# Optimization experiments

Measured on AMD Instinct MI355X. Metric: run time of the kernel, lower is better.

## Reference

```python
import jax, jax.numpy as jnp
import numpy as np

N = 100000   # nodes
E = 3200000  # edges (avg degree 32)
D = 128      # input feature dim


def setup_inputs() -> dict:
    key = jax.random.key(0)
    ks = jax.random.split(key, 9)
    x = jax.random.normal(ks[0], (N, D), dtype=jnp.float32)
    edge_index = jax.random.randint(ks[1], (2, E), 0, N, dtype=jnp.int32)
    s = 0.05
    W1 = jax.random.normal(ks[2], (D, 64), dtype=jnp.float32) * s
    b1 = jnp.zeros((64,), dtype=jnp.float32)
    W2 = jax.random.normal(ks[3], (64, 32), dtype=jnp.float32) * s
    b2 = jnp.zeros((32,), dtype=jnp.float32)
    Wfc = jax.random.normal(ks[4], (32, 1), dtype=jnp.float32) * s
    bfc = jnp.zeros((1,), dtype=jnp.float32)
    return {"x": x, "edge_index": edge_index, "W1": W1, "b1": b1,
            "W2": W2, "b2": b2, "Wfc": Wfc, "bfc": bfc}


def _gcn_layer(x, W, b, src, dst, n):
    # GCNConv: h = D^{-1/2} (A + I) D^{-1/2} (x W) + b
    h = x @ W  # [n, out]
    loop = jnp.arange(n, dtype=src.dtype)
    src2 = jnp.concatenate([src, loop])  # add self-loops
    dst2 = jnp.concatenate([dst, loop])
    deg = jax.ops.segment_sum(jnp.ones_like(dst2, dtype=h.dtype), dst2,
                              num_segments=n)  # >= 1 due to self-loops
    dis = jax.lax.rsqrt(deg)
    norm = dis[src2] * dis[dst2]  # [E+n]
    msgs = h[src2] * norm[:, None]  # gather + scale
    return jax.ops.segment_sum(msgs, dst2, num_segments=n) + b


def reference(x, edge_index, W1, b1, W2, b2, Wfc, bfc):
    src, dst = edge_index[0], edge_index[1]
    n = x.shape[0]
    h = jax.nn.relu(_gcn_layer(x, W1, b1, src, dst, n))
    h = jax.nn.relu(_gcn_layer(h, W2, b2, src, dst, n))
    return h @ Wfc + bfc  # [n, 1]
```

## Files before the change

kernel.cpp:

```cpp
#include <hip/hip_runtime.h>
#include <hip/hip_bf16.h>
#include <hip/hip_fp16.h>


#define SCAN_CHUNK 1024
#define BSHIFT 7
#define BSIZE 128
#define B1 256
#define CSR_CAP 5120

__device__ inline void f4fma(float4& a, float s, const float4& b) {
    a.x = fmaf(s, b.x, a.x); a.y = fmaf(s, b.y, a.y);
    a.z = fmaf(s, b.z, a.z); a.w = fmaf(s, b.w, a.w);
}
__device__ inline void f4add(float4& a, const float4& b) {
    a.x += b.x; a.y += b.y; a.z += b.z; a.w += b.w;
}
__device__ inline void f4red(float4& a, int off) {
    a.x += __shfl_xor(a.x, off); a.y += __shfl_xor(a.y, off);
    a.z += __shfl_xor(a.z, off); a.w += __shfl_xor(a.w, off);
}
__device__ inline void h8load(const __half* p, float4& a, float4& b) {
    uint4 r = *(const uint4*)p;
    __half2* h = (__half2*)&r;
    float2 f0 = __half22float2(h[0]);
    float2 f1 = __half22float2(h[1]);
    float2 f2 = __half22float2(h[2]);
    float2 f3 = __half22float2(h[3]);
    a = make_float4(f0.x, f0.y, f1.x, f1.y);
    b = make_float4(f2.x, f2.y, f3.x, f3.y);
}
__device__ inline void hacc2(unsigned h, float& x, float& y) {
    asm("v_fma_mix_f32 %0, %2, %3, %0 op_sel:[0,0,0] op_sel_hi:[1,0,0]\n\t"
        "v_fma_mix_f32 %1, %2, %3, %1 op_sel:[1,0,0] op_sel_hi:[1,0,0]"
        : "+v"(x), "+v"(y)
        : "v"(h), "v"(1.0f));
}
__device__ inline void h8acc(const __half* p, float4& a, float4& b) {
    uint4 r = *(const uint4*)p;
    hacc2(r.x, a.x, a.y);
    hacc2(r.y, a.z, a.w);
    hacc2(r.z, b.x, b.y);
    hacc2(r.w, b.z, b.w);
}
__device__ inline void h4store(__half* p, float4 v) {
    __half2 a = __floats2half2_rn(v.x, v.y);
    __half2 b = __floats2half2_rn(v.z, v.w);
    uint2 r; r.x = *(uint*)&a; r.y = *(uint*)&b;
    *(uint2*)p = r;
}

__global__ void k_gscan1(const int* __restrict__ in, int* __restrict__ part, int m) {
    int t = threadIdx.x;
    int base = blockIdx.x * SCAN_CHUNK + t * 4;
    int s = 0;
    for (int u = 0; u < 4; ++u) { int i = base + u; if (i < m) s += in[i]; }
    for (int o = 32; o; o >>= 1) s += __shfl_down(s, o);
    __shared__ int ws[4];
    if ((t & 63) == 0) ws[t >> 6] = s;
    __syncthreads();
    if (t == 0) part[blockIdx.x] = ws[0] + ws[1] + ws[2] + ws[3];
}

__global__ void k_gscan2(const int* __restrict__ in, const int* __restrict__ part,
                         int* __restrict__ out, int m, int nblk) {
    int t = threadIdx.x;
    int b = blockIdx.x;
    int pv = (t < b && t < nblk) ? part[t] : 0;
    int ps = pv;
    for (int o = 32; o; o >>= 1) ps += __shfl_down(ps, o);
    __shared__ int sh[4];
    if ((t & 63) == 0) sh[t >> 6] = ps;
    __syncthreads();
    int blockoff = sh[0] + sh[1] + sh[2] + sh[3];

    int base = b * SCAN_CHUNK + t * 4;
    int v0 = 0, v1 = 0, v2 = 0, v3 = 0;
    if (base + 0 < m) v0 = in[base + 0];
    if (base + 1 < m) v1 = in[base + 1];
    if (base + 2 < m) v2 = in[base + 2];
    if (base + 3 < m) v3 = in[base + 3];
    int tot = v0 + v1 + v2 + v3;
    int lane = t & 63, wid = t >> 6;
    int incl = tot;
    for (int o = 1; o < 64; o <<= 1) { int u = __shfl_up(incl, o); if (lane >= o) incl += u; }
    int excl = incl - tot;
    __shared__ int wt[4];
    if (lane == 63) wt[wid] = incl;
    __syncthreads();
    int woff = 0;
    for (int w = 0; w < wid; ++w) woff += wt[w];
    int off = blockoff + woff + excl;
    if (base + 0 < m) out[base + 0] = off;
    if (base + 1 < m) out[base + 1] = off + v0;
    if (base + 2 < m) out[base + 2] = off + v0 + v1;
    if (base + 3 < m) out[base + 3] = off + v0 + v1 + v2;
}

__global__ __launch_bounds__(256) void k_hist(const int* __restrict__ dst,
                                              int* __restrict__ ghist,
                                              int e, int echunk, int nbuck) {
    extern __shared__ int h[];
    int t = threadIdx.x, b = blockIdx.x;
    for (int i = t; i < nbuck; i += 256) h[i] = 0;
    __syncthreads();
    int s = b * echunk, epd = min(e, s + echunk);
    for (int i = s + t * 4; i < epd; i += 1024) {
        if (i + 3 < epd) {
            int4 d4 = *(const int4*)&dst[i];
            atomicAdd(&h[d4.x >> BSHIFT], 1);
            atomicAdd(&h[d4.y >> BSHIFT], 1);
            atomicAdd(&h[d4.z >> BSHIFT], 1);
            atomicAdd(&h[d4.w >> BSHIFT], 1);
        } else {
            for (int u = i; u < epd; ++u) atomicAdd(&h[dst[u] >> BSHIFT], 1);
        }
    }
    __syncthreads();
    for (int k = t; k < nbuck; k += 256)
        ghist[k * B1 + b] = h[k];
}

__global__ __launch_bounds__(256) void k_binscatter(
        const int* __restrict__ src, const int* __restrict__ dst,
        const int* __restrict__ ghist_s, int* __restrict__ ebuf,
        int e, int echunk, int nbuck) {
    extern __shared__ int cur[];
    int t = threadIdx.x, b = blockIdx.x;
    for (int k = t; k < nbuck; k += 256)
        cur[k] = ghist_s[k * B1 + b];
    __syncthreads();
    int s = b * echunk, epd = min(e, s + echunk);
    for (int i = s + t * 4; i < epd; i += 1024) {
        if (i + 3 < epd) {
            int4 d4 = *(const int4*)&dst[i];
            int4 s4 = *(const int4*)&src[i];
            int p0 = atomicAdd(&cur[d4.x >> BSHIFT], 1);
            int p1 = atomicAdd(&cur[d4.y >> BSHIFT], 1);
            int p2 = atomicAdd(&cur[d4.z >> BSHIFT], 1);
            int p3 = atomicAdd(&cur[d4.w >> BSHIFT], 1);
            ebuf[p0] = (s4.x << BSHIFT) | (d4.x & (BSIZE - 1));
            ebuf[p1] = (s4.y << BSHIFT) | (d4.y & (BSIZE - 1));
            ebuf[p2] = (s4.z << BSHIFT) | (d4.z & (BSIZE - 1));
            ebuf[p3] = (s4.w << BSHIFT) | (d4.w & (BSIZE - 1));
        } else {
            for (int u = i; u < epd; ++u) {
                int d = dst[u];
                int pos = atomicAdd(&cur[d >> BSHIFT], 1);
                ebuf[pos] = (src[u] << BSHIFT) | (d & (BSIZE - 1));
            }
        }
    }
}

__global__ __launch_bounds__(256) void k_csr(
        const int* __restrict__ ebuf, const int* __restrict__ ghist_s,
        int* __restrict__ ebuf2, int* __restrict__ rowptr, int* __restrict__ degi,
        float* __restrict__ dis, int n, int e, int nbuck) {
    int k = blockIdx.x, t = threadIdx.x;
    int estart = ghist_s[k * B1];
    int eend = (k + 1 < nbuck) ? ghist_s[(k + 1) * B1] : e;
    int ecnt = eend - estart;
    __shared__ int ein[CSR_CAP];
    __shared__ int eout[CSR_CAP];
    __shared__ int cnt[BSIZE];
    __shared__ int cur[BSIZE];
    __shared__ int wt[4];
    if (t < BSIZE) cnt[t] = 0;
    bool staged = (ecnt <= CSR_CAP);
    if (staged) {
        for (int i = t; i < ecnt; i += 256) ein[i] = ebuf[estart + i];
    }
    __syncthreads();
    if (staged) {
        for (int i = t; i < ecnt; i += 256)
            atomicAdd(&cnt[ein[i] & (BSIZE - 1)], 1);
    } else {
        for (int i = estart + t; i < eend; i += 256)
            atomicAdd(&cnt[ebuf[i] & (BSIZE - 1)], 1);
    }
    __syncthreads();
    int v = (t < BSIZE) ? cnt[t] : 0;
    int lane = t & 63, wid = t >> 6;
    int incl = v;
    for (int o = 1; o < 64; o <<= 1) { int u = __shfl_up(incl, o); if (lane >= o) incl += u; }
    if (lane == 63) wt[wid] = incl;
    __syncthreads();
    int woff = (wid == 1) ? wt[0] : 0;
    int excl = woff + incl - v;
    if (t < BSIZE) {
        cur[t] = excl;
        int node = k * BSIZE + t;
        if (node < n) {
            rowptr[node] = estart + excl;
            degi[node]   = v;
            dis[node]    = rsqrtf((float)(v + 1));
        }
    }
    __syncthreads();
    if (staged) {
        for (int i = t; i < ecnt; i += 256) {
            int w = ein[i];
            int pos = atomicAdd(&cur[w & (BSIZE - 1)], 1);
            eout[pos] = w;
        }
        __syncthreads();
        for (int i = t; i < ecnt; i += 256)
            ebuf2[estart + i] = eout[i];
    } else {
        for (int i = estart + t; i < eend; i += 256) {
            int w = ebuf[i];
            int pos = estart + atomicAdd(&cur[w & (BSIZE - 1)], 1);
            ebuf2[pos] = w;
        }
    }
}

#define SA 132
__global__ __launch_bounds__(256) void k_gemm1(
        const float* __restrict__ x, const float* __restrict__ W1,
        const float* __restrict__ dis, __half* __restrict__ h1s, int n) {
    __shared__ float Xs[64 * SA];
    __shared__ float Ws[128 * 64];
    int t = threadIdx.x;
    int nbase = blockIdx.x * 64;
    for (int i = t; i < 2048; i += 256)
        ((float4*)Ws)[i] = ((const float4*)W1)[i];
    for (int i = t; i < 2048; i += 256) {
        int row = i >> 5, q = i & 31;
        int r = nbase + row; if (r >= n) r = n - 1;
        float4 v = ((const float4*)(x + (size_t)r * 128))[q];
        *(float4*)&Xs[row * SA + q * 4] = v;
    }
    __syncthreads();
    int wid = t >> 6, lane = t & 63;
    int lx = lane & 7, ly = lane >> 3;
    int wm = wid & 1, wn = wid >> 1;
    int row0 = wm * 32 + ly * 4;
    int col0 = wn * 32 + lx * 4;
    float4 acc0 = {0.f,0.f,0.f,0.f}, acc1 = acc0, acc2 = acc0, acc3 = acc0;
#pragma unroll 4
    for (int k4 = 0; k4 < 32; ++k4) {
        int k = k4 * 4;
        float4 a0 = *(const float4*)&Xs[(row0 + 0) * SA + k];
        float4 a1 = *(const float4*)&Xs[(row0 + 1) * SA + k];
        float4 a2 = *(const float4*)&Xs[(row0 + 2) * SA + k];
        float4 a3 = *(const float4*)&Xs[(row0 + 3) * SA + k];
        float4 b0 = *(const float4*)&Ws[(k + 0) * 64 + col0];
        float4 b1 = *(const float4*)&Ws[(k + 1) * 64 + col0];
        float4 b2 = *(const float4*)&Ws[(k + 2) * 64 + col0];
        float4 b3 = *(const float4*)&Ws[(k + 3) * 64 + col0];
        f4fma(acc0, a0.x, b0); f4fma(acc0, a0.y, b1); f4fma(acc0, a0.z, b2); f4fma(acc0, a0.w, b3);
        f4fma(acc1, a1.x, b0); f4fma(acc1, a1.y, b1); f4fma(acc1, a1.z, b2); f4fma(acc1, a1.w, b3);
        f4fma(acc2, a2.x, b0); f4fma(acc2, a2.y, b1); f4fma(acc2, a2.z, b2); f4fma(acc2, a2.w, b3);
        f4fma(acc3, a3.x, b0); f4fma(acc3, a3.y, b1); f4fma(acc3, a3.z, b2); f4fma(acc3, a3.w, b3);
    }
    int grow = nbase + row0;
#pragma unroll
    for (int r = 0; r < 4; ++r) {
        int rr = grow + r;
        if (rr < n) {
            float d = dis[rr];
            float4 o = (r == 0) ? acc0 : (r == 1) ? acc1 : (r == 2) ? acc2 : acc3;
            o.x *= d; o.y *= d; o.z *= d; o.w *= d;
            h4store(&h1s[(size_t)rr * 64 + col0], o);
        }
    }
}

__global__ __launch_bounds__(256) void k_agg12(
        const __half* __restrict__ h1s, const int* __restrict__ ents,
        const int* __restrict__ rowptr, const int* __restrict__ degi,
        const float* __restrict__ dis, const float* __restrict__ b1,
        const float* __restrict__ W2, __half* __restrict__ h2s, int n) {
    __shared__ float h1row[4][72];
    int wid = threadIdx.x >> 6, lane = threadIdx.x & 63;
    int v = blockIdx.x * 4 + wid;
    int vc = min(v, n - 1);
    int start = rowptr[vc], cnt = degi[vc];
    int eg = lane >> 3;
    int fq = (lane & 7) * 8;
    int c = lane & 31, hh = lane >> 5;
    float w2r[32];
#pragma unroll
    for (int j = 0; j < 32; ++j)
        w2r[j] = W2[(hh * 32 + j) * 32 + c];
    float4 accA = {0.f, 0.f, 0.f, 0.f}, accB = accA;
    if (cnt > 0 && cnt <= 64) {
        int pre = ents[start + min(lane, cnt - 1)];
        int ng = cnt >> 3;
#pragma unroll 4
        for (int g = 0; g < ng; ++g) {
            unsigned s = ((unsigned)__shfl(pre, g * 8 + eg)) >> BSHIFT;
            h8acc(&h1s[(size_t)s * 64 + fq], accA, accB);
        }
        int rem = cnt & 7, j0 = cnt & ~7;
        if (rem) {
            unsigned s = ((unsigned)__shfl(pre, j0 + (eg < rem ? eg : 0))) >> BSHIFT;
            float4 a, b; h8load(&h1s[(size_t)s * 64 + fq], a, b);
            if (eg < rem) { f4add(accA, a); f4add(accB, b); }
        }
    } else if (cnt > 64) {
        int j = 0;
        for (; j + 8 <= cnt; j += 8) {
            unsigned s = ((unsigned)ents[start + j + eg]) >> BSHIFT;
            h8acc(&h1s[(size_t)s * 64 + fq], accA, accB);
        }
        int rem = cnt - j;
        if (rem) {
            unsigned s = ((unsigned)ents[start + j + (eg < rem ? eg : 0)]) >> BSHIFT;
            float4 a, b; h8load(&h1s[(size_t)s * 64 + fq], a, b);
            if (eg < rem) { f4add(accA, a); f4add(accB, b); }
        }
    }
    if (eg == 0) {
        h8acc(&h1s[(size_t)vc * 64 + fq], accA, accB);
    }
    f4red(accA, 8);  f4red(accB, 8);
    f4red(accA, 16); f4red(accB, 16);
    f4red(accA, 32); f4red(accB, 32);
    float d = dis[vc];
    if (eg == 0) {
        float4 bq0 = *(const float4*)&b1[fq];
        float4 bq1 = *(const float4*)&b1[fq + 4];
        float4 o0, o1;
        o0.x = fmaxf(fmaf(d, accA.x, bq0.x), 0.f);
        o0.y = fmaxf(fmaf(d, accA.y, bq0.y), 0.f);
        o0.z = fmaxf(fmaf(d, accA.z, bq0.z), 0.f);
        o0.w = fmaxf(fmaf(d, accA.w, bq0.w), 0.f);
        o1.x = fmaxf(fmaf(d, accB.x, bq1.x), 0.f);
        o1.y = fmaxf(fmaf(d, accB.y, bq1.y), 0.f);
        o1.z = fmaxf(fmaf(d, accB.z, bq1.z), 0.f);
        o1.w = fmaxf(fmaf(d, accB.w, bq1.w), 0.f);
        *(float4*)&h1row[wid][fq] = o0;
        *(float4*)&h1row[wid][fq + 4] = o1;
    }
    __syncthreads();
    float p = 0.f;
#pragma unroll
    for (int j = 0; j < 32; j += 4) {
        float4 hv = *(const float4*)&h1row[wid][hh * 32 + j];
        p = fmaf(hv.x, w2r[j + 0], p);
        p = fmaf(hv.y, w2r[j + 1], p);
        p = fmaf(hv.z, w2r[j + 2], p);
        p = fmaf(hv.w, w2r[j + 3], p);
    }
    p += __shfl_xor(p, 32);
    if (hh == 0 && v < n) h2s[(size_t)v * 32 + c] = __float2half(p * d);
}

__global__ void k_agg2(const __half* __restrict__ h2s, const int* __restrict__ ents,
                       const int* __restrict__ rowptr, const int* __restrict__ degi,
                       const float* __restrict__ dis, const float* __restrict__ b2,
                       const float* __restrict__ Wfc, const float* __restrict__ bfc,
                       float* __restrict__ out, int n) {
    int wid = threadIdx.x >> 6, lane = threadIdx.x & 63;
    int v = blockIdx.x * 4 + wid;
    if (v >= n) return;
    int start = rowptr[v], cnt = degi[v];
    int eg = lane >> 2;
    int fq = (lane & 3) * 8;
    float4 accA = {0.f, 0.f, 0.f, 0.f}, accB = accA;
    if (cnt > 0 && cnt <= 64) {
        int pre = ents[start + min(lane, cnt - 1)];
        int ng = cnt >> 4;
#pragma unroll 4
        for (int g = 0; g < ng; ++g) {
            unsigned s = ((unsigned)__shfl(pre, g * 16 + eg)) >> BSHIFT;
            h8acc(&h2s[(size_t)s * 32 + fq], accA, accB);
        }
        int rem = cnt & 15, j0 = cnt & ~15;
        if (rem) {
            unsigned s = ((unsigned)__shfl(pre, j0 + (eg < rem ? eg : 0))) >> BSHIFT;
            float4 a, b; h8load(&h2s[(size_t)s * 32 + fq], a, b);
            if (eg < rem) { f4add(accA, a); f4add(accB, b); }
        }
    } else if (cnt > 64) {
        int j = 0;
        for (; j + 16 <= cnt; j += 16) {
            unsigned s = ((unsigned)ents[start + j + eg]) >> BSHIFT;
            h8acc(&h2s[(size_t)s * 32 + fq], accA, accB);
        }
        int rem = cnt - j;
        if (rem) {
            unsigned s = ((unsigned)ents[start + j + (eg < rem ? eg : 0)]) >> BSHIFT;
            float4 a, b; h8load(&h2s[(size_t)s * 32 + fq], a, b);
            if (eg < rem) { f4add(accA, a); f4add(accB, b); }
        }
    }
    if (eg == 0) {
        h8acc(&h2s[(size_t)v * 32 + fq], accA, accB);
    }
    f4red(accA, 4);  f4red(accB, 4);
    f4red(accA, 8);  f4red(accB, 8);
    f4red(accA, 16); f4red(accB, 16);
    f4red(accA, 32); f4red(accB, 32);
    float p = 0.f;
    if (eg == 0) {
        float d = dis[v];
        float4 bq0 = *(const float4*)&b2[fq];
        float4 bq1 = *(const float4*)&b2[fq + 4];
        float4 wq0 = *(const float4*)&Wfc[fq];
        float4 wq1 = *(const float4*)&Wfc[fq + 4];
        p  = fmaxf(fmaf(d, accA.x, bq0.x), 0.f) * wq0.x;
        p += fmaxf(fmaf(d, accA.y, bq0.y), 0.f) * wq0.y;
        p += fmaxf(fmaf(d, accA.z, bq0.z), 0.f) * wq0.z;
        p += fmaxf(fmaf(d, accA.w, bq0.w), 0.f) * wq0.w;
        p += fmaxf(fmaf(d, accB.x, bq1.x), 0.f) * wq1.x;
        p += fmaxf(fmaf(d, accB.y, bq1.y), 0.f) * wq1.y;
        p += fmaxf(fmaf(d, accB.z, bq1.z), 0.f) * wq1.z;
        p += fmaxf(fmaf(d, accB.w, bq1.w), 0.f) * wq1.w;
    }
    p += __shfl_xor(p, 1); p += __shfl_xor(p, 2);
    if (lane == 0) out[v] = p + bfc[0];
}

extern "C" void kernel_launch(void* const* d_in, const int* in_sizes, int n_in,
                              void* d_out, int out_size, void* d_ws, size_t ws_size,
                              hipStream_t stream) {
    const float* x   = (const float*)d_in[0];
    const int*   ei  = (const int*)d_in[1];
    const float* W1  = (const float*)d_in[2];
    const float* b1  = (const float*)d_in[3];
    const float* W2  = (const float*)d_in[4];
    const float* b2  = (const float*)d_in[5];
    const float* Wfc = (const float*)d_in[6];
    const float* bfc = (const float*)d_in[7];
    float* out = (float*)d_out;

    const int n = in_sizes[0] / 128;
    const int e = in_sizes[1] / 2;
    const int* src = ei;
    const int* dst = ei + e;

    const int nbuck = (n + BSIZE - 1) / BSIZE;
    const int m = nbuck * B1;
    const int echunk = (e + B1 - 1) / B1;

    char* p = (char*)d_ws;
    size_t off = 0;
    auto carve = [&](size_t bytes) { void* r = p + off; off = (off + bytes + 255) & ~(size_t)255; return r; };
    int*   ghist   = (int*)  carve((size_t)m * 4);
    int*   ghist_s = (int*)  carve((size_t)m * 4);
    int*   part    = (int*)  carve(256 * 4);
    float* dis     = (float*)carve((size_t)n * 4);
    int*   rowptr  = (int*)  carve((size_t)n * 4);
    int*   degi    = (int*)  carve((size_t)n * 4);
    int*   ebuf2   = (int*)  carve((size_t)e * 4);
    __half* h2s    = (__half*)carve((size_t)n * 32 * 2);
    void*  ebuf_or_h1s = carve((size_t)e * 4);
    int*    ebuf = (int*)ebuf_or_h1s;
    __half* h1s  = (__half*)ebuf_or_h1s;
    (void)ws_size;

    const int nblk_scan = (m + SCAN_CHUNK - 1) / SCAN_CHUNK;
    const size_t lds_buck = (size_t)nbuck * 4;

    k_hist<<<B1, 256, lds_buck, stream>>>(dst, ghist, e, echunk, nbuck);
    k_gscan1<<<nblk_scan, 256, 0, stream>>>(ghist, part, m);
    k_gscan2<<<nblk_scan, 256, 0, stream>>>(ghist, part, ghist_s, m, nblk_scan);
    k_binscatter<<<B1, 256, lds_buck, stream>>>(src, dst, ghist_s, ebuf, e, echunk, nbuck);
    k_csr<<<nbuck, 256, 0, stream>>>(ebuf, ghist_s, ebuf2, rowptr, degi, dis, n, e, nbuck);
    k_gemm1<<<(n + 63) / 64, 256, 0, stream>>>(x, W1, dis, h1s, n);
    k_agg12<<<(n + 3) / 4, 256, 0, stream>>>(h1s, ebuf2, rowptr, degi, dis, b1, W2, h2s, n);
    k_agg2<<<(n + 3) / 4, 256, 0, stream>>>(h2s, ebuf2, rowptr, degi, dis, b2, Wfc, bfc, out, n);
}
```

Baseline: 305.6 us.

## Replace bucketed two-pass CSR build with global atomic degree count and scatter

Removes the LDS-bucketed histogram, bin-scatter and per-bucket CSR sort kernels. In their place it counts per-node degree with global atomics, scans it directly into rowptr, cursors and dis, and scatters source ids into CSR slots with global atomics. Entries now hold plain source ids, so the aggregation kernels drop the shift decode, and W2 is pre-transposed so agg12 can load its weights as vectorized float4. This cuts kernel count and passes over the edges but relies on heavily contended global atomics with random destinations and gives a nondeterministic neighbor order within each row.

Measured after the change: 699.0 us. +128.7%, slower.

```diff
diff --git a/kernel.cpp b/kernel.cpp
--- a/kernel.cpp
+++ b/kernel.cpp
@@ -4,10 +4,6 @@
 
 
 #define SCAN_CHUNK 1024
-#define BSHIFT 7
-#define BSIZE 128
-#define B1 256
-#define CSR_CAP 5120
 
 __device__ inline void f4fma(float4& a, float s, const float4& b) {
     a.x = fmaf(s, b.x, a.x); a.y = fmaf(s, b.y, a.y);
@@ -50,6 +46,28 @@
     *(uint2*)p = r;
 }
 
+__global__ __launch_bounds__(256) void k_deg(const int* __restrict__ dst,
+                                             int* __restrict__ deg,
+                                             const float* __restrict__ W2,
+                                             float* __restrict__ W2T, int e) {
+    int tid = blockIdx.x * 256 + threadIdx.x;
+    int i = tid * 4;
+    int stride = gridDim.x * 1024;
+    for (; i + 3 < e; i += stride) {
+        int4 d4 = *(const int4*)&dst[i];
+        atomicAdd(&deg[d4.x], 1);
+        atomicAdd(&deg[d4.y], 1);
+        atomicAdd(&deg[d4.z], 1);
+        atomicAdd(&deg[d4.w], 1);
+    }
+    for (int u = (e & ~3) + tid; u < e; u += gridDim.x * 256)
+        atomicAdd(&deg[dst[u]], 1);
+    if (blockIdx.x == 0) {
+        for (int j = threadIdx.x; j < 2048; j += 256)
+            W2T[j] = W2[(j & 63) * 32 + (j >> 6)];
+    }
+}
+
 __global__ void k_gscan1(const int* __restrict__ in, int* __restrict__ part, int m) {
     int t = threadIdx.x;
     int base = blockIdx.x * SCAN_CHUNK + t * 4;
@@ -63,7 +81,8 @@
 }
 
 __global__ void k_gscan2(const int* __restrict__ in, const int* __restrict__ part,
-                         int* __restrict__ out, int m, int nblk) {
+                         int* __restrict__ rowptr, int* __restrict__ cur,
+                         float* __restrict__ dis, int m, int nblk) {
     int t = threadIdx.x;
     int b = blockIdx.x;
     int pv = (t < b && t < nblk) ? part[t] : 0;
@@ -91,129 +110,28 @@
     int woff = 0;
     for (int w = 0; w < wid; ++w) woff += wt[w];
     int off = blockoff + woff + excl;
-    if (base + 0 < m) out[base + 0] = off;
-    if (base + 1 < m) out[base + 1] = off + v0;
-    if (base + 2 < m) out[base + 2] = off + v0 + v1;
-    if (base + 3 < m) out[base + 3] = off + v0 + v1 + v2;
-}
-
-__global__ __launch_bounds__(256) void k_hist(const int* __restrict__ dst,
-                                              int* __restrict__ ghist,
-                                              int e, int echunk, int nbuck) {
-    extern __shared__ int h[];
-    int t = threadIdx.x, b = blockIdx.x;
-    for (int i = t; i < nbuck; i += 256) h[i] = 0;
-    __syncthreads();
-    int s = b * echunk, epd = min(e, s + echunk);
-    for (int i = s + t * 4; i < epd; i += 1024) {
-        if (i + 3 < epd) {
-            int4 d4 = *(const int4*)&dst[i];
-            atomicAdd(&h[d4.x >> BSHIFT], 1);
-            atomicAdd(&h[d4.y >> BSHIFT], 1);
-            atomicAdd(&h[d4.z >> BSHIFT], 1);
-            atomicAdd(&h[d4.w >> BSHIFT], 1);
-        } else {
-            for (int u = i; u < epd; ++u) atomicAdd(&h[dst[u] >> BSHIFT], 1);
-        }
-    }
-    __syncthreads();
-    for (int k = t; k < nbuck; k += 256)
-        ghist[k * B1 + b] = h[k];
-}
-
-__global__ __launch_bounds__(256) void k_binscatter(
+    if (base + 0 < m) { rowptr[base+0] = off;          cur[base+0] = off;          dis[base+0] = rsqrtf((float)(v0+1)); }
+    if (base + 1 < m) { int o1 = off+v0;               rowptr[base+1] = o1; cur[base+1] = o1; dis[base+1] = rsqrtf((float)(v1+1)); }
+    if (base + 2 < m) { int o2 = off+v0+v1;            rowptr[base+2] = o2; cur[base+2] = o2; dis[base+2] = rsqrtf((float)(v2+1)); }
+    if (base + 3 < m) { int o3 = off+v0+v1+v2;         rowptr[base+3] = o3; cur[base+3] = o3; dis[base+3] = rsqrtf((float)(v3+1)); }
+}
+
+__global__ __launch_bounds__(256) void k_scatter(
         const int* __restrict__ src, const int* __restrict__ dst,
-        const int* __restrict__ ghist_s, int* __restrict__ ebuf,
-        int e, int echunk, int nbuck) {
-    extern __shared__ int cur[];
-    int t = threadIdx.x, b = blockIdx.x;
-    for (int k = t; k < nbuck; k += 256)
-        cur[k] = ghist_s[k * B1 + b];
-    __syncthreads();
-    int s = b * echunk, epd = min(e, s + echunk);
-    for (int i = s + t * 4; i < epd; i += 1024) {
-        if (i + 3 < epd) {
-            int4 d4 = *(const int4*)&dst[i];
-            int4 s4 = *(const int4*)&src[i];
-            int p0 = atomicAdd(&cur[d4.x >> BSHIFT], 1);
-            int p1 = atomicAdd(&cur[d4.y >> BSHIFT], 1);
-            int p2 = atomicAdd(&cur[d4.z >> BSHIFT], 1);
-            int p3 = atomicAdd(&cur[d4.w >> BSHIFT], 1);
-            ebuf[p0] = (s4.x << BSHIFT) | (d4.x & (BSIZE - 1));
-            ebuf[p1] = (s4.y << BSHIFT) | (d4.y & (BSIZE - 1));
-            ebuf[p2] = (s4.z << BSHIFT) | (d4.z & (BSIZE - 1));
-            ebuf[p3] = (s4.w << BSHIFT) | (d4.w & (BSIZE - 1));
-        } else {
-            for (int u = i; u < epd; ++u) {
-                int d = dst[u];
-                int pos = atomicAdd(&cur[d >> BSHIFT], 1);
-                ebuf[pos] = (src[u] << BSHIFT) | (d & (BSIZE - 1));
-            }
-        }
-    }
-}
-
-__global__ __launch_bounds__(256) void k_csr(
-        const int* __restrict__ ebuf, const int* __restrict__ ghist_s,
-        int* __restrict__ ebuf2, int* __restrict__ rowptr, int* __restrict__ degi,
-        float* __restrict__ dis, int n, int e, int nbuck) {
-    int k = blockIdx.x, t = threadIdx.x;
-    int estart = ghist_s[k * B1];
-    int eend = (k + 1 < nbuck) ? ghist_s[(k + 1) * B1] : e;
-    int ecnt = eend - estart;
-    __shared__ int ein[CSR_CAP];
-    __shared__ int eout[CSR_CAP];
-    __shared__ int cnt[BSIZE];
-    __shared__ int cur[BSIZE];
-    __shared__ int wt[4];
-    if (t < BSIZE) cnt[t] = 0;
-    bool staged = (ecnt <= CSR_CAP);
-    if (staged) {
-        for (int i = t; i < ecnt; i += 256) ein[i] = ebuf[estart + i];
-    }
-    __syncthreads();
-    if (staged) {
-        for (int i = t; i < ecnt; i += 256)
-            atomicAdd(&cnt[ein[i] & (BSIZE - 1)], 1);
-    } else {
-        for (int i = estart + t; i < eend; i += 256)
-            atomicAdd(&cnt[ebuf[i] & (BSIZE - 1)], 1);
-    }
-    __syncthreads();
-    int v = (t < BSIZE) ? cnt[t] : 0;
-    int lane = t & 63, wid = t >> 6;
-    int incl = v;
-    for (int o = 1; o < 64; o <<= 1) { int u = __shfl_up(incl, o); if (lane >= o) incl += u; }
-    if (lane == 63) wt[wid] = incl;
-    __syncthreads();
-    int woff = (wid == 1) ? wt[0] : 0;
-    int excl = woff + incl - v;
-    if (t < BSIZE) {
-        cur[t] = excl;
-        int node = k * BSIZE + t;
-        if (node < n) {
-            rowptr[node] = estart + excl;
-            degi[node]   = v;
-            dis[node]    = rsqrtf((float)(v + 1));
-        }
-    }
-    __syncthreads();
-    if (staged) {
-        for (int i = t; i < ecnt; i += 256) {
-            int w = ein[i];
-            int pos = atomicAdd(&cur[w & (BSIZE - 1)], 1);
-            eout[pos] = w;
-        }
-        __syncthreads();
-        for (int i = t; i < ecnt; i += 256)
-            ebuf2[estart + i] = eout[i];
-    } else {
-        for (int i = estart + t; i < eend; i += 256) {
-            int w = ebuf[i];
-            int pos = estart + atomicAdd(&cur[w & (BSIZE - 1)], 1);
-            ebuf2[pos] = w;
-        }
-    }
+        int* __restrict__ cur, int* __restrict__ ents, int e) {
+    int tid = blockIdx.x * 256 + threadIdx.x;
+    int i = tid * 4;
+    int stride = gridDim.x * 1024;
+    for (; i + 3 < e; i += stride) {
+        int4 s4 = *(const int4*)&src[i];
+        int4 d4 = *(const int4*)&dst[i];
+        ents[atomicAdd(&cur[d4.x], 1)] = s4.x;
+        ents[atomicAdd(&cur[d4.y], 1)] = s4.y;
+        ents[atomicAdd(&cur[d4.z], 1)] = s4.z;
+        ents[atomicAdd(&cur[d4.w], 1)] = s4.w;
+    }
+    for (int u = (e & ~3) + tid; u < e; u += gridDim.x * 256)
+        ents[atomicAdd(&cur[dst[u]], 1)] = src[u];
 }
 
 #define SA 132
@@ -270,45 +188,48 @@
 
 __global__ __launch_bounds__(256) void k_agg12(
         const __half* __restrict__ h1s, const int* __restrict__ ents,
-        const int* __restrict__ rowptr, const int* __restrict__ degi,
+        const int* __restrict__ rowptr, const int* __restrict__ deg,
         const float* __restrict__ dis, const float* __restrict__ b1,
-        const float* __restrict__ W2, __half* __restrict__ h2s, int n) {
+        const float* __restrict__ W2T, __half* __restrict__ h2s, int n) {
     __shared__ float h1row[4][72];
     int wid = threadIdx.x >> 6, lane = threadIdx.x & 63;
     int v = blockIdx.x * 4 + wid;
     int vc = min(v, n - 1);
-    int start = rowptr[vc], cnt = degi[vc];
+    int start = rowptr[vc], cnt = deg[vc];
     int eg = lane >> 3;
     int fq = (lane & 7) * 8;
     int c = lane & 31, hh = lane >> 5;
     float w2r[32];
+    {
+        const float4* wtp = (const float4*)&W2T[(size_t)c * 64 + hh * 32];
 #pragma unroll
-    for (int j = 0; j < 32; ++j)
-        w2r[j] = W2[(hh * 32 + j) * 32 + c];
+        for (int q = 0; q < 8; ++q)
+            *(float4*)&w2r[q * 4] = wtp[q];
+    }
     float4 accA = {0.f, 0.f, 0.f, 0.f}, accB = accA;
     if (cnt > 0 && cnt <= 64) {
         int pre = ents[start + min(lane, cnt - 1)];
         int ng = cnt >> 3;
 #pragma unroll 4
         for (int g = 0; g < ng; ++g) {
-            unsigned s = ((unsigned)__shfl(pre, g * 8 + eg)) >> BSHIFT;
+            unsigned s = (unsigned)__shfl(pre, g * 8 + eg);
             h8acc(&h1s[(size_t)s * 64 + fq], accA, accB);
         }
         int rem = cnt & 7, j0 = cnt & ~7;
         if (rem) {
-            unsigned s = ((unsigned)__shfl(pre, j0 + (eg < rem ? eg : 0))) >> BSHIFT;
+            unsigned s = (unsigned)__shfl(pre, j0 + (eg < rem ? eg : 0));
             float4 a, b; h8load(&h1s[(size_t)s * 64 + fq], a, b);
             if (eg < rem) { f4add(accA, a); f4add(accB, b); }
         }
     } else if (cnt > 64) {
         int j = 0;
         for (; j + 8 <= cnt; j += 8) {
-            unsigned s = ((unsigned)ents[start + j + eg]) >> BSHIFT;
+            unsigned s = (unsigned)ents[start + j + eg];
             h8acc(&h1s[(size_t)s * 64 + fq], accA, accB);
         }
         int rem = cnt - j;
         if (rem) {
-            unsigned s = ((unsigned)ents[start + j + (eg < rem ? eg : 0)]) >> BSHIFT;
+            unsigned s = (unsigned)ents[start + j + (eg < rem ? eg : 0)];
             float4 a, b; h8load(&h1s[(size_t)s * 64 + fq], a, b);
             if (eg < rem) { f4add(accA, a); f4add(accB, b); }
         }
@@ -350,14 +271,14 @@
 }
 
 __global__ void k_agg2(const __half* __restrict__ h2s, const int* __restrict__ ents,
-                       const int* __restrict__ rowptr, const int* __restrict__ degi,
+                       const int* __restrict__ rowptr, const int* __restrict__ deg,
                        const float* __restrict__ dis, const float* __restrict__ b2,
                        const float* __restrict__ Wfc, const float* __restrict__ bfc,
                        float* __restrict__ out, int n) {
     int wid = threadIdx.x >> 6, lane = threadIdx.x & 63;
     int v = blockIdx.x * 4 + wid;
     if (v >= n) return;
-    int start = rowptr[v], cnt = degi[v];
+    int start = rowptr[v], cnt = deg[v];
     int eg = lane >> 2;
     int fq = (lane & 3) * 8;
     float4 accA = {0.f, 0.f, 0.f, 0.f}, accB = accA;
@@ -366,24 +287,24 @@
         int ng = cnt >> 4;
 #pragma unroll 4
         for (int g = 0; g < ng; ++g) {
-            unsigned s = ((unsigned)__shfl(pre, g * 16 + eg)) >> BSHIFT;
+            unsigned s = (unsigned)__shfl(pre, g * 16 + eg);
             h8acc(&h2s[(size_t)s * 32 + fq], accA, accB);
         }
         int rem = cnt & 15, j0 = cnt & ~15;
         if (rem) {
-            unsigned s = ((unsigned)__shfl(pre, j0 + (eg < rem ? eg : 0))) >> BSHIFT;
+            unsigned s = (unsigned)__shfl(pre, j0 + (eg < rem ? eg : 0));
             float4 a, b; h8load(&h2s[(size_t)s * 32 + fq], a, b);
             if (eg < rem) { f4add(accA, a); f4add(accB, b); }
         }
     } else if (cnt > 64) {
         int j = 0;
         for (; j + 16 <= cnt; j += 16) {
-            unsigned s = ((unsigned)ents[start + j + eg]) >> BSHIFT;
+            unsigned s = (unsigned)ents[start + j + eg];
             h8acc(&h2s[(size_t)s * 32 + fq], accA, accB);
         }
         int rem = cnt - j;
         if (rem) {
-            unsigned s = ((unsigned)ents[start + j + (eg < rem ? eg : 0)]) >> BSHIFT;
+            unsigned s = (unsigned)ents[start + j + (eg < rem ? eg : 0)];
             float4 a, b; h8load(&h2s[(size_t)s * 32 + fq], a, b);
             if (eg < rem) { f4add(accA, a); f4add(accB, b); }
         }
@@ -433,35 +354,29 @@
     const int* src = ei;
     const int* dst = ei + e;
 
-    const int nbuck = (n + BSIZE - 1) / BSIZE;
-    const int m = nbuck * B1;
-    const int echunk = (e + B1 - 1) / B1;
-
     char* p = (char*)d_ws;
     size_t off = 0;
     auto carve = [&](size_t bytes) { void* r = p + off; off = (off + bytes + 255) & ~(size_t)255; return r; };
-    int*   ghist   = (int*)  carve((size_t)m * 4);
-    int*   ghist_s = (int*)  carve((size_t)m * 4);
+    int*   deg     = (int*)  carve((size_t)n * 4);
+    int*   rowptr  = (int*)  carve((size_t)n * 4);
+    int*   cur     = (int*)  carve((size_t)n * 4);
+    float* dis     = (float*)carve((size_t)n * 4);
     int*   part    = (int*)  carve(256 * 4);
-    float* dis     = (float*)carve((size_t)n * 4);
-    int*   rowptr  = (int*)  carve((size_t)n * 4);
-    int*   degi    = (int*)  carve((size_t)n * 4);
+    float* W2T     = (float*)carve(2048 * 4);
     int*   ebuf2   = (int*)  carve((size_t)e * 4);
     __half* h2s    = (__half*)carve((size_t)n * 32 * 2);
-    void*  ebuf_or_h1s = carve((size_t)e * 4);
-    int*    ebuf = (int*)ebuf_or_h1s;
-    __half* h1s  = (__half*)ebuf_or_h1s;
+    __half* h1s    = (__half*)carve((size_t)n * 64 * 2);
     (void)ws_size;
 
-    const int nblk_scan = (m + SCAN_CHUNK - 1) / SCAN_CHUNK;
-    const size_t lds_buck = (size_t)nbuck * 4;
-
-    k_hist<<<B1, 256, lds_buck, stream>>>(dst, ghist, e, echunk, nbuck);
-    k_gscan1<<<nblk_scan, 256, 0, stream>>>(ghist, part, m);
-    k_gscan2<<<nblk_scan, 256, 0, stream>>>(ghist, part, ghist_s, m, nblk_scan);
-    k_binscatter<<<B1, 256, lds_buck, stream>>>(src, dst, ghist_s, ebuf, e, echunk, nbuck);
-    k_csr<<<nbuck, 256, 0, stream>>>(ebuf, ghist_s, ebuf2, rowptr, degi, dis, n, e, nbuck);
+    const int nblk_scan = (n + SCAN_CHUNK - 1) / SCAN_CHUNK;
+    const int nblk_e = (e / 4 + 255) / 256;
+
+    hipMemsetAsync(deg, 0, (size_t)n * 4, stream);
+    k_deg<<<nblk_e, 256, 0, stream>>>(dst, deg, W2, W2T, e);
+    k_gscan1<<<nblk_scan, 256, 0, stream>>>(deg, part, n);
+    k_gscan2<<<nblk_scan, 256, 0, stream>>>(deg, part, rowptr, cur, dis, n, nblk_scan);
+    k_scatter<<<nblk_e, 256, 0, stream>>>(src, dst, cur, ebuf2, e);
     k_gemm1<<<(n + 63) / 64, 256, 0, stream>>>(x, W1, dis, h1s, n);
-    k_agg12<<<(n + 3) / 4, 256, 0, stream>>>(h1s, ebuf2, rowptr, degi, dis, b1, W2, h2s, n);
-    k_agg2<<<(n + 3) / 4, 256, 0, stream>>>(h2s, ebuf2, rowptr, degi, dis, b2, Wfc, bfc, out, n);
-}
+    k_agg12<<<(n + 3) / 4, 256, 0, stream>>>(h1s, ebuf2, rowptr, deg, dis, b1, W2T, h2s, n);
+    k_agg2<<<(n + 3) / 4, 256, 0, stream>>>(h2s, ebuf2, rowptr, deg, dis, b2, Wfc, bfc, out, n);
+}
```
